# Kernel tuning notes

Hardware: AMD Instinct MI355X
Metric: run time of the kernel (lower is better)

The kernel has to match this reference:

```python
import jax, jax.numpy as jnp
import numpy as np

B, T, H, W = 2, 4, 32, 32
DINO_DIM, COG_DIM, NUM_HEADS = 768, 1920, 12
HEAD_DIM = DINO_DIM // NUM_HEADS


def _layernorm(x, g, b, eps=1e-5):
    mu = jnp.mean(x, axis=-1, keepdims=True)
    var = jnp.mean(jnp.square(x - mu), axis=-1, keepdims=True)
    return (x - mu) * jax.lax.rsqrt(var + eps) * g + b


def setup_inputs() -> dict:
    key = jax.random.key(0)
    ks = jax.random.split(key, 12)
    s_d = 1.0 / np.sqrt(DINO_DIM)
    s_c = 1.0 / np.sqrt(COG_DIM)
    return {
        "dino_query": jax.random.normal(ks[0], (B, DINO_DIM, H, W), jnp.float32),
        "cogvideo_keys": jax.random.normal(ks[1], (B, T, H, W, COG_DIM), jnp.float32),
        "temporal_weights": jax.random.uniform(ks[2], (T,), jnp.float32),
        "Wq": jax.random.normal(ks[3], (DINO_DIM, DINO_DIM), jnp.float32) * s_d,
        "bq": jnp.zeros((DINO_DIM,), jnp.float32),
        "Wk": jax.random.normal(ks[4], (COG_DIM, DINO_DIM), jnp.float32) * s_c,
        "bk": jnp.zeros((DINO_DIM,), jnp.float32),
        "Wv": jax.random.normal(ks[5], (COG_DIM, DINO_DIM), jnp.float32) * s_c,
        "bv": jnp.zeros((DINO_DIM,), jnp.float32),
        "Wo": jax.random.normal(ks[6], (DINO_DIM, DINO_DIM), jnp.float32) * s_d,
        "bo": jnp.zeros((DINO_DIM,), jnp.float32),
        "gq": jnp.ones((DINO_DIM,), jnp.float32),
        "Bq": jnp.zeros((DINO_DIM,), jnp.float32),
        "gkv": jnp.ones((COG_DIM,), jnp.float32),
        "Bkv": jnp.zeros((COG_DIM,), jnp.float32),
    }


def reference(dino_query, cogvideo_keys, temporal_weights,
              Wq, bq, Wk, bk, Wv, bv, Wo, bo, gq, Bq, gkv, Bkv):
    b, c, h, w = dino_query.shape
    t = cogvideo_keys.shape[1]
    hw, tkv = h * w, t * cogvideo_keys.shape[2] * cogvideo_keys.shape[3]

    # [B,C,H,W] -> [B,H,W,C]; project after LayerNorm
    xq = _layernorm(jnp.transpose(dino_query, (0, 2, 3, 1)), gq, Bq)
    xkv = _layernorm(cogvideo_keys, gkv, Bkv)
    q = xq @ Wq + bq                      # [B,H,W,C]
    k = xkv @ Wk + bk                     # [B,T,Hk,Wk,C]
    v = xkv @ Wv + bv

    q = q.reshape(b, hw, NUM_HEADS, HEAD_DIM).transpose(0, 2, 1, 3)    # [B,nh,HW,hd]
    k = k.reshape(b, tkv, NUM_HEADS, HEAD_DIM).transpose(0, 2, 1, 3)   # [B,nh,TKV,hd]
    v = v.reshape(b, tkv, NUM_HEADS, HEAD_DIM).transpose(0, 2, 1, 3)

    scores = jnp.einsum('bnqd,bnkd->bnqk', q, k) / np.sqrt(HEAD_DIM)   # [B,nh,HW,TKV]
    # per-key temporal weight: each of the T frames contributes HW keys
    w_key = jnp.repeat(temporal_weights, tkv // t)                     # [TKV]
    scores = scores * w_key[None, None, None, :]
    probs = jax.nn.softmax(scores, axis=-1)

    out = jnp.einsum('bnqk,bnkd->bnqd', probs, v)                      # [B,nh,HW,hd]
    out = out.transpose(0, 2, 1, 3).reshape(b, h, w, c)
    out = out @ Wo + bo
    return jnp.transpose(out, (0, 3, 1, 2))                            # [B,C,H,W]
```

## Files before the change

### kernel.cpp

```cpp
#include <hip/hip_runtime.h>
#include <hip/hip_bf16.h>
#include <math.h>

#define BB   2
#define HWl  1024
#define DINO 768
#define COG  1920
#define NHh  12
#define TKV  4096
#define MQ   (BB*HWl)
#define MKV  (BB*TKV)
#define NSPL 4
#define ROWS_PER_SPLIT (BB*NHh*HWl)

typedef __attribute__((ext_vector_type(8))) short bf16x8;
typedef __attribute__((ext_vector_type(4))) float f32x4;

__device__ __forceinline__ unsigned short f2bf_bits(float f) {
    __hip_bfloat16 h = __float2bfloat16(f);
    return *reinterpret_cast<unsigned short*>(&h);
}

__device__ __forceinline__ void glds16(const __hip_bfloat16* g, __hip_bfloat16* l) {
    __builtin_amdgcn_global_load_lds((const __attribute__((address_space(1))) void*)g,
                                     (__attribute__((address_space(3))) void*)l, 16, 0, 0);
}

__global__ __launch_bounds__(256) void prep1(const float* __restrict__ dino,
                                             const float* __restrict__ cog,
                                             const float* __restrict__ gkv, const float* __restrict__ Bkv,
                                             const float* __restrict__ Wq, const float* __restrict__ Wk,
                                             const float* __restrict__ Wv, const float* __restrict__ Wo,
                                             float* __restrict__ xqT,
                                             __hip_bfloat16* __restrict__ xkv,
                                             __hip_bfloat16* WqT, __hip_bfloat16* WkvT, __hip_bfloat16* WoT) {
    int bid = blockIdx.x, tid = threadIdx.x;
    if (bid < 2048) {
        const int W = COG, W4 = W >> 2, NC = 8;
        int row = bid * 4 + (tid >> 6), lane = tid & 63;
        const float4* xr = (const float4*)(cog + (size_t)row * W);
        const float4* g4 = (const float4*)gkv;
        const float4* b4 = (const float4*)Bkv;
        float4 v[NC];
        float s = 0.f, ss = 0.f;
        #pragma unroll
        for (int i = 0; i < NC; ++i) {
            int c = lane + i * 64;
            float4 t = (c < W4) ? xr[c] : (float4){0.f, 0.f, 0.f, 0.f};
            v[i] = t;
            s  += t.x + t.y + t.z + t.w;
            ss += t.x * t.x + t.y * t.y + t.z * t.z + t.w * t.w;
        }
        #pragma unroll
        for (int off = 1; off < 64; off <<= 1) {
            s  += __shfl_xor(s, off);
            ss += __shfl_xor(ss, off);
        }
        float mu = s / W;
        float rstd = rsqrtf(ss / W - mu * mu + 1e-5f);
        ushort4* yr = (ushort4*)(xkv + (size_t)row * W);
        #pragma unroll
        for (int i = 0; i < NC; ++i) {
            int c = lane + i * 64;
            if (c < W4) {
                float4 t = v[i];
                float4 gg = g4[c], bb = b4[c];
                ushort4 o;
                o.x = f2bf_bits((t.x - mu) * rstd * gg.x + bb.x);
                o.y = f2bf_bits((t.y - mu) * rstd * gg.y + bb.y);
                o.z = f2bf_bits((t.z - mu) * rstd * gg.z + bb.z);
                o.w = f2bf_bits((t.w - mu) * rstd * gg.w + bb.w);
                yr[c] = o;
            }
        }
    } else if (bid < 2432) {
        int t = bid - 2048;
        int h0 = (t & 15) * 64;
        int c0 = ((t >> 4) % 12) * 64;
        int b = t / 192;
        __shared__ float T[64][65];
        #pragma unroll
        for (int i = 0; i < 16; ++i) {
            int idx = tid + i * 256;
            int c = idx >> 6, h = idx & 63;
            T[c][h] = dino[((size_t)b * DINO + c0 + c) * HWl + h0 + h];
        }
        __syncthreads();
        #pragma unroll
        for (int i = 0; i < 16; ++i) {
            int idx = tid + i * 256;
            int r = idx >> 6, c = idx & 63;
            xqT[((size_t)b * HWl + h0 + r) * DINO + c0 + c] = T[c][r];
        }
    } else {
        int bid2 = bid - 2432;
        int mid = bid2 / 1440, r = bid2 % 1440;
        int k0 = (r % 60) * 32, n0 = (r / 60) * 32;
        const float* src = (mid == 0) ? Wq : (mid == 1) ? Wk : (mid == 2) ? Wv : Wo;
        __hip_bfloat16* dst;
        int rowoff = 0;
        if (mid == 0) dst = WqT;
        else if (mid == 1) dst = WkvT;
        else if (mid == 2) { dst = WkvT; rowoff = 768; }
        else dst = WoT;
        int K = (mid == 1 || mid == 2) ? COG : DINO;
        if (k0 >= K) return;
        __shared__ float T[32][33];
        #pragma unroll
        for (int i = 0; i < 4; ++i) {
            int idx = tid + i * 256;
            int rr = idx >> 5, c = idx & 31;
            T[rr][c] = src[(size_t)(k0 + rr) * DINO + n0 + c];
        }
        __syncthreads();
        #pragma unroll
        for (int i = 0; i < 4; ++i) {
            int idx = tid + i * 256;
            int rr = idx >> 5, c = idx & 31;
            dst[(size_t)(rowoff + n0 + rr) * K + k0 + c] = __float2bfloat16(T[c][rr]);
        }
    }
}

__global__ __launch_bounds__(256) void prep2(const float* __restrict__ x,
                                             const float* __restrict__ g,
                                             const float* __restrict__ be,
                                             __hip_bfloat16* __restrict__ y) {
    const int W = DINO, NC = 3;
    int row = blockIdx.x * 4 + (threadIdx.x >> 6);
    int lane = threadIdx.x & 63;
    const float4* xr = (const float4*)(x + (size_t)row * W);
    const float4* g4 = (const float4*)g;
    const float4* b4 = (const float4*)be;
    float4 v[NC];
    float s = 0.f, ss = 0.f;
    #pragma unroll
    for (int i = 0; i < NC; ++i) {
        int c = lane + i * 64;
        float4 t = xr[c];
        v[i] = t;
        s  += t.x + t.y + t.z + t.w;
        ss += t.x * t.x + t.y * t.y + t.z * t.z + t.w * t.w;
    }
    #pragma unroll
    for (int off = 1; off < 64; off <<= 1) {
        s  += __shfl_xor(s, off);
        ss += __shfl_xor(ss, off);
    }
    float mu = s / W;
    float rstd = rsqrtf(ss / W - mu * mu + 1e-5f);
    ushort4* yr = (ushort4*)(y + (size_t)row * W);
    #pragma unroll
    for (int i = 0; i < NC; ++i) {
        int c = lane + i * 64;
        float4 t = v[i];
        float4 gg = g4[c], bb = b4[c];
        ushort4 o;
        o.x = f2bf_bits((t.x - mu) * rstd * gg.x + bb.x);
        o.y = f2bf_bits((t.y - mu) * rstd * gg.y + bb.y);
        o.z = f2bf_bits((t.z - mu) * rstd * gg.z + bb.z);
        o.w = f2bf_bits((t.w - mu) * rstd * gg.w + bb.w);
        yr[c] = o;
    }
}

#define VM4 asm volatile("s_waitcnt vmcnt(4)" ::: "memory")
#define VM0 asm volatile("s_waitcnt vmcnt(0)" ::: "memory")

#define STAGE_A(d, h, tau) do { \
    int _o = (aRow + (h) * 64) * Kd + (tau) * 64 + cgo; \
    __hip_bfloat16* _dp = SM + (d) * 32768 + (h) * 8192 + wido; \
    glds16(Ag + _o, _dp); \
    glds16(Ag + _o + 128 * Kd, _dp + 4096); \
} while (0)

#define STAGE_B(d, h, tau) do { \
    int _o = (bRow + (h) * 32) * Kd + (tau) * 64 + cgo; \
    __hip_bfloat16* _dp = SM + (d) * 32768 + 16384 + (h) * 8192 + wido; \
    glds16(Bg + _o, _dp); \
    glds16(Bg + _o + 128 * Kd, _dp + 4096); \
} while (0)

#define PHASE(MH, NH, STAGE_STMT, WAIT_STMT) do { \
    const __hip_bfloat16* _Ab = SM + cur * 32768 + (MH) * 8192 + aoff; \
    const __hip_bfloat16* _Bb = SM + cur * 32768 + 16384 + (NH) * 8192 + boff; \
    bf16x8 _a[4][2], _b[2][2]; \
    _Pragma("unroll") \
    for (int i = 0; i < 4; ++i) { \
        _a[i][0] = *(const bf16x8*)(_Ab + i * 1024 + c0); \
        _a[i][1] = *(const bf16x8*)(_Ab + i * 1024 + c1); \
    } \
    _Pragma("unroll") \
    for (int j = 0; j < 2; ++j) { \
        _b[j][0] = *(const bf16x8*)(_Bb + j * 1024 + c0); \
        _b[j][1] = *(const bf16x8*)(_Bb + j * 1024 + c1); \
    } \
    STAGE_STMT; \
    WAIT_STMT; \
    __builtin_amdgcn_sched_barrier(0); \
    __builtin_amdgcn_s_barrier(); \
    __builtin_amdgcn_sched_barrier(0); \
    __builtin_amdgcn_s_setprio(1); \
    _Pragma("unroll") \
    for (int i = 0; i < 4; ++i) \
        _Pragma("unroll") \
        for (int j = 0; j < 2; ++j) { \
            f32x4 _t = acc[(MH) * 4 + i][(NH) * 2 + j]; \
            _t = __builtin_amdgcn_mfma_f32_16x16x32_bf16(_a[i][0], _b[j][0], _t, 0, 0, 0); \
            _t = __builtin_amdgcn_mfma_f32_16x16x32_bf16(_a[i][1], _b[j][1], _t, 0, 0, 0); \
            acc[(MH) * 4 + i][(NH) * 2 + j] = _t; \
        } \
    __builtin_amdgcn_s_setprio(0); \
    __builtin_amdgcn_sched_barrier(0); \
    __builtin_amdgcn_s_barrier(); \
} while (0)

__global__ __launch_bounds__(512, 2) void stage1(const __hip_bfloat16* __restrict__ xq,
                                                 const __hip_bfloat16* __restrict__ WqT,
                                                 const float* __restrict__ bq,
                                                 __hip_bfloat16* __restrict__ qb,
                                                 const __hip_bfloat16* __restrict__ xkv,
                                                 const __hip_bfloat16* __restrict__ WkvT,
                                                 const float* __restrict__ bk,
                                                 const float* __restrict__ bv,
                                                 __hip_bfloat16* __restrict__ kb,
                                                 __hip_bfloat16* __restrict__ VT) {
    __shared__ __hip_bfloat16 SM[65536];
    int bid = blockIdx.x;
    int tid = threadIdx.x;
    int wid = tid >> 6, lane = tid & 63;
    int l4 = lane & 15, lq = lane >> 4;
    int wr = wid >> 2, wc = wid & 3;
    int tr = tid >> 3;
    int cgo = ((tid & 7) ^ (tr & 7)) * 8;
    int wido = wid * 512;

    const __hip_bfloat16 *Ag, *Bg;
    int m0, n0, Kd, NT, isQ;
    if (bid < 192) {
        m0 = (bid & 31) * 256; n0 = (bid >> 5) * 256;
        Ag = xkv; Bg = WkvT; Kd = COG; NT = COG / 64; isQ = 0;
    } else {
        int t = bid - 192;
        m0 = (t & 7) * 256; n0 = (t >> 3) * 256;
        Ag = xq; Bg = WqT; Kd = DINO; NT = DINO / 64; isQ = 1;
    }

    const int aRow = m0 + tr;
    const int bRow = n0 + ((tid >> 8) << 6) + (tr & 31);
    const int aoff = (wr * 64 + l4) * 64;
    const int boff = (wc * 32 + l4) * 64;
    const int c0 = ((lq) ^ (l4 & 7)) * 8;
    const int c1 = ((4 + lq) ^ (l4 & 7)) * 8;

    f32x4 acc[8][4];
    #pragma unroll
    for (int i = 0; i < 8; ++i)
        #pragma unroll
        for (int j = 0; j < 4; ++j) acc[i][j] = (f32x4){0.f, 0.f, 0.f, 0.f};

    STAGE_A(0, 0, 0); STAGE_B(0, 0, 0); STAGE_A(0, 1, 0); STAGE_B(0, 1, 0);
    STAGE_A(1, 0, 1); STAGE_B(1, 0, 1);
    VM4;
    __builtin_amdgcn_s_barrier();

    for (int g = 0; g < NT; ++g) {
        int cur = g & 1, nxt = cur ^ 1;
        bool s1 = (g + 1 < NT), s2 = (g + 2 < NT);
        PHASE(0, 0, if (s1) STAGE_A(nxt, 1, g + 1), (void)0);
        PHASE(1, 0, if (s1) STAGE_B(nxt, 1, g + 1), (void)0);
        PHASE(0, 1, if (s2) STAGE_B(cur, 0, g + 2), (void)0);
        PHASE(1, 1, if (s2) STAGE_A(cur, 0, g + 2),
              if (s2) { VM4; } else { VM0; });
    }

    if (isQ) {
        #pragma unroll
        for (int ii = 0; ii < 8; ++ii)
            #pragma unroll
            for (int jj = 0; jj < 4; ++jj) {
                int m = m0 + wr * 128 + (ii >> 2) * 64 + (ii & 3) * 16 + lq * 4;
                int n = n0 + wc * 64 + (jj >> 1) * 32 + (jj & 1) * 16 + l4;
                float bb = bq[n];
                #pragma unroll
                for (int r = 0; r < 4; ++r)
                    qb[(size_t)(m + r) * DINO + n] = __float2bfloat16(acc[ii][jj][r] + bb);
            }
    } else if (n0 < 768) {
        #pragma unroll
        for (int ii = 0; ii < 8; ++ii)
            #pragma unroll
            for (int jj = 0; jj < 4; ++jj) {
                int m = m0 + wr * 128 + (ii >> 2) * 64 + (ii & 3) * 16 + lq * 4;
                int n = n0 + wc * 64 + (jj >> 1) * 32 + (jj & 1) * 16 + l4;
                float bb = bk[n];
                #pragma unroll
                for (int r = 0; r < 4; ++r)
                    kb[(size_t)(m + r) * DINO + n] = __float2bfloat16(acc[ii][jj][r] + bb);
            }
    } else {
        #pragma unroll
        for (int ii = 0; ii < 8; ++ii)
            #pragma unroll
            for (int jj = 0; jj < 4; ++jj) {
                int m = m0 + wr * 128 + (ii >> 2) * 64 + (ii & 3) * 16 + lq * 4;
                int nv = n0 - 768 + wc * 64 + (jj >> 1) * 32 + (jj & 1) * 16 + l4;
                float bb = bv[nv];
                #pragma unroll
                for (int r = 0; r < 4; ++r) {
                    int mm = m + r;
                    VT[((size_t)((mm >> 12) * 768 + nv)) * TKV + (mm & 4095)] =
                        __float2bfloat16(acc[ii][jj][r] + bb);
                }
            }
    }
}

__global__ __launch_bounds__(256) void gemm_o(const __hip_bfloat16* __restrict__ A,
                                              const __hip_bfloat16* __restrict__ Bt,
                                              const float* __restrict__ bias,
                                              float* __restrict__ out) {
    const int K = DINO;
    __shared__ __hip_bfloat16 As[64 * 64];
    __shared__ __hip_bfloat16 Bs[64 * 64];
    int m0 = blockIdx.x * 64, n0 = blockIdx.y * 64;
    int tid = threadIdx.x, w = tid >> 6, lane = tid & 63;
    int l4 = lane & 15, lq = lane >> 4;
    int mq = (w & 1) * 32, nq = (w >> 1) * 32;
    f32x4 acc[2][2];
    #pragma unroll
    for (int i = 0; i < 2; ++i)
        #pragma unroll
        for (int j = 0; j < 2; ++j) acc[i][j] = (f32x4){0.f, 0.f, 0.f, 0.f};

    int rr = tid >> 3;
    int gc = (tid & 7) ^ (rr & 7);
    const __hip_bfloat16* ag = A  + (size_t)(m0 + rr) * K + gc * 8;
    const __hip_bfloat16* bg = Bt + (size_t)(n0 + rr) * K + gc * 8;
    __hip_bfloat16* asl = As + (w * 8) * 64;
    __hip_bfloat16* bsl = Bs + (w * 8) * 64;
    int sws = l4 & 7;

    for (int k0 = 0; k0 < K; k0 += 64) {
        __syncthreads();
        #pragma unroll
        for (int g = 0; g < 2; ++g) {
            glds16(ag + (size_t)(g * 32) * K + k0, asl + g * 32 * 64);
            glds16(bg + (size_t)(g * 32) * K + k0, bsl + g * 32 * 64);
        }
        __syncthreads();
        #pragma unroll
        for (int h = 0; h < 2; ++h) {
            bf16x8 a[2], b[2];
            #pragma unroll
            for (int i = 0; i < 2; ++i)
                a[i] = *(const bf16x8*)(As + (mq + 16 * i + l4) * 64 + (((h * 4 + lq) ^ sws) * 8));
            #pragma unroll
            for (int j = 0; j < 2; ++j)
                b[j] = *(const bf16x8*)(Bs + (nq + 16 * j + l4) * 64 + (((h * 4 + lq) ^ sws) * 8));
            #pragma unroll
            for (int i = 0; i < 2; ++i)
                #pragma unroll
                for (int j = 0; j < 2; ++j)
                    acc[i][j] = __builtin_amdgcn_mfma_f32_16x16x32_bf16(b[j], a[i], acc[i][j], 0, 0, 0);
        }
    }
    #pragma unroll
    for (int i = 0; i < 2; ++i)
        #pragma unroll
        for (int j = 0; j < 2; ++j)
            #pragma unroll
            for (int r = 0; r < 4; ++r) {
                int n = n0 + nq + 16 * j + lq * 4 + r;
                int m = m0 + mq + 16 * i + l4;
                int b = m >> 10, hw = m & 1023;
                out[((size_t)b * DINO + n) * HWl + hw] = acc[i][j][r] + bias[n];
            }
}

__global__ __launch_bounds__(256) void attn4(const __hip_bfloat16* __restrict__ qb,
                                             const __hip_bfloat16* __restrict__ kb,
                                             const __hip_bfloat16* __restrict__ VT,
                                             const float* __restrict__ tw,
                                             __hip_bfloat16* __restrict__ Opart,
                                             float* __restrict__ lpart) {
    int bid = blockIdx.x;
    int g = bid % 96, qc = bid / 96;
    int s = g & 3, bh = g >> 2;
    int head = bh % NHh, b = bh / NHh;
    int tid = threadIdx.x, w = tid >> 6, lane = tid & 63;
    int l4 = lane & 15, lq = lane >> 4;

    __shared__ __hip_bfloat16 Ks[2 * 64 * 64];
    __shared__ __hip_bfloat16 Vs[2 * 64 * 64];
    __shared__ __hip_bfloat16 Ps[4 * 32 * 64];

    const __hip_bfloat16* qbase = qb + (size_t)(b * HWl + qc * 128 + w * 32 + l4) * DINO + head * 64;
    bf16x8 qA0 = *(const bf16x8*)(qbase + lq * 8);
    bf16x8 qA1 = *(const bf16x8*)(qbase + 32 + lq * 8);
    const __hip_bfloat16* qbase2 = qbase + (size_t)16 * DINO;
    bf16x8 qB0 = *(const bf16x8*)(qbase2 + lq * 8);
    bf16x8 qB1 = *(const bf16x8*)(qbase2 + 32 + lq * 8);

    float c = tw[s] * 0.125f * 1.44269504f;
    float l_iA = 0.f, l_iB = 0.f;
    f32x4 oA[4], oB[4];
    #pragma unroll
    for (int j = 0; j < 4; ++j) { oA[j] = (f32x4){0.f,0.f,0.f,0.f}; oB[j] = (f32x4){0.f,0.f,0.f,0.f}; }

    int rowA = w * 16 + (lane >> 3);
    int cg = (lane & 7) ^ ((lane >> 3) & 7);
    const __hip_bfloat16* kg0 = kb + (size_t)(b * TKV + s * 1024 + rowA) * DINO + head * 64 + cg * 8;
    const __hip_bfloat16* kg1 = kg0 + (size_t)8 * DINO;
    const __hip_bfloat16* vg0 = VT + (size_t)(b * 768 + head * 64 + rowA) * TKV + s * 1024 + cg * 8;
    const __hip_bfloat16* vg1 = vg0 + (size_t)8 * TKV;
    int klo0 = (w * 2 + 0) * 512, klo1 = (w * 2 + 1) * 512;

    int sw0 = (lq ^ (l4 & 7)) * 8;
    int sw1 = ((4 + lq) ^ (l4 & 7)) * 8;
    __hip_bfloat16* PsA = Ps + w * 2048 + l4 * 64;
    __hip_bfloat16* PsB = Ps + w * 2048 + (16 + l4) * 64;

    glds16(kg0, Ks + klo0);
    glds16(kg1, Ks + klo1);
    glds16(vg0, Vs + klo0);
    glds16(vg1, Vs + klo1);

    for (int kt = 0; kt < 16; ++kt) {
        int cur = (kt & 1) * 4096;
        __syncthreads();
        if (kt < 15) {
            int nxt = cur ^ 4096;
            glds16(kg0 + (size_t)(kt + 1) * 64 * DINO, Ks + nxt + klo0);
            glds16(kg1 + (size_t)(kt + 1) * 64 * DINO, Ks + nxt + klo1);
            glds16(vg0 + (kt + 1) * 64, Vs + nxt + klo0);
            glds16(vg1 + (kt + 1) * 64, Vs + nxt + klo1);
        }
        const __hip_bfloat16* Kc = Ks + cur;
        const __hip_bfloat16* Vc = Vs + cur;

        f32x4 stA[4], stB[4];
        #pragma unroll
        for (int j = 0; j < 4; ++j) {
            const __hip_bfloat16* kr = Kc + (16 * j + l4) * 64;
            bf16x8 kf0 = *(const bf16x8*)(kr + sw0);
            bf16x8 kf1 = *(const bf16x8*)(kr + sw1);
            f32x4 a = (f32x4){0.f,0.f,0.f,0.f};
            a = __builtin_amdgcn_mfma_f32_16x16x32_bf16(kf0, qA0, a, 0, 0, 0);
            a = __builtin_amdgcn_mfma_f32_16x16x32_bf16(kf1, qA1, a, 0, 0, 0);
            stA[j] = a;
            f32x4 bb = (f32x4){0.f,0.f,0.f,0.f};
            bb = __builtin_amdgcn_mfma_f32_16x16x32_bf16(kf0, qB0, bb, 0, 0, 0);
            bb = __builtin_amdgcn_mfma_f32_16x16x32_bf16(kf1, qB1, bb, 0, 0, 0);
            stB[j] = bb;
        }

        float lsA = 0.f, lsB = 0.f;
        #pragma unroll
        for (int j = 0; j < 4; ++j)
            #pragma unroll
            for (int r = 0; r < 4; ++r) {
                float eA = exp2f(stA[j][r] * c);
                float eB = exp2f(stB[j][r] * c);
                stA[j][r] = eA; lsA += eA;
                stB[j][r] = eB; lsB += eB;
            }
        lsA += __shfl_xor(lsA, 16); lsA += __shfl_xor(lsA, 32);
        lsB += __shfl_xor(lsB, 16); lsB += __shfl_xor(lsB, 32);
        l_iA += lsA; l_iB += lsB;

        #pragma unroll
        for (int j = 0; j < 4; ++j) {
            int off = (((2 * j + (lq >> 1)) ^ (l4 & 7)) << 3) + (lq & 1) * 4;
            ushort4 pA, pB;
            pA.x = f2bf_bits(stA[j][0]); pA.y = f2bf_bits(stA[j][1]);
            pA.z = f2bf_bits(stA[j][2]); pA.w = f2bf_bits(stA[j][3]);
            pB.x = f2bf_bits(stB[j][0]); pB.y = f2bf_bits(stB[j][1]);
            pB.z = f2bf_bits(stB[j][2]); pB.w = f2bf_bits(stB[j][3]);
            *(ushort4*)&PsA[off] = pA;
            *(ushort4*)&PsB[off] = pB;
        }
        bf16x8 paA0 = *(const bf16x8*)(PsA + sw0);
        bf16x8 paA1 = *(const bf16x8*)(PsA + sw1);
        bf16x8 paB0 = *(const bf16x8*)(PsB + sw0);
        bf16x8 paB1 = *(const bf16x8*)(PsB + sw1);

        #pragma unroll
        for (int j = 0; j < 4; ++j) {
            const __hip_bfloat16* vr = Vc + (16 * j + l4) * 64;
            bf16x8 vf0 = *(const bf16x8*)(vr + sw0);
            bf16x8 vf1 = *(const bf16x8*)(vr + sw1);
            oA[j] = __builtin_amdgcn_mfma_f32_16x16x32_bf16(paA0, vf0, oA[j], 0, 0, 0);
            oA[j] = __builtin_amdgcn_mfma_f32_16x16x32_bf16(paA1, vf1, oA[j], 0, 0, 0);
            oB[j] = __builtin_amdgcn_mfma_f32_16x16x32_bf16(paB0, vf0, oB[j], 0, 0, 0);
            oB[j] = __builtin_amdgcn_mfma_f32_16x16x32_bf16(paB1, vf1, oB[j], 0, 0, 0);
        }
    }

    size_t rb = (size_t)s * ROWS_PER_SPLIT + (size_t)(b * NHh + head) * HWl + qc * 128 + w * 32;
    #pragma unroll
    for (int j = 0; j < 4; ++j)
        #pragma unroll
        for (int r = 0; r < 4; ++r) {
            Opart[(rb + lq * 4 + r) * 64 + j * 16 + l4]      = __float2bfloat16(oA[j][r]);
            Opart[(rb + 16 + lq * 4 + r) * 64 + j * 16 + l4] = __float2bfloat16(oB[j][r]);
        }
    if (lq == 0) {
        lpart[rb + l4]      = l_iA;
        lpart[rb + 16 + l4] = l_iB;
    }
}

__global__ void combine(const __hip_bfloat16* __restrict__ Opart, const float* __restrict__ lpart,
                        __hip_bfloat16* __restrict__ attn) {
    int p = blockIdx.x * 4 + (threadIdx.x >> 6);
    int d = threadIdx.x & 63;
    float L = 0.f, O = 0.f;
    #pragma unroll
    for (int s = 0; s < NSPL; ++s) {
        L += lpart[(size_t)s * ROWS_PER_SPLIT + p];
        O += __bfloat162float(Opart[((size_t)s * ROWS_PER_SPLIT + p) * 64 + d]);
    }
    float res = O / L;
    int q = p & 1023;
    int bh = p >> 10;
    int head = bh % NHh, b = bh / NHh;
    attn[((size_t)(b * HWl + q)) * DINO + head * 64 + d] = __float2bfloat16(res);
}

extern "C" void kernel_launch(void* const* d_in, const int* in_sizes, int n_in,
                              void* d_out, int out_size, void* d_ws, size_t ws_size,
                              hipStream_t stream) {
    (void)in_sizes; (void)n_in; (void)out_size; (void)ws_size;
    const float* dino = (const float*)d_in[0];
    const float* cog  = (const float*)d_in[1];
    const float* tw   = (const float*)d_in[2];
    const float* Wq   = (const float*)d_in[3];
    const float* bq   = (const float*)d_in[4];
    const float* Wk   = (const float*)d_in[5];
    const float* bk   = (const float*)d_in[6];
    const float* Wv   = (const float*)d_in[7];
    const float* bv   = (const float*)d_in[8];
    const float* Wo   = (const float*)d_in[9];
    const float* bo   = (const float*)d_in[10];
    const float* gq   = (const float*)d_in[11];
    const float* Bq   = (const float*)d_in[12];
    const float* gkv  = (const float*)d_in[13];
    const float* Bkv  = (const float*)d_in[14];

    char* p = (char*)d_ws;
    float* xqT = (float*)p;                    p += (size_t)MQ * DINO * 4;
    __hip_bfloat16* xq = (__hip_bfloat16*)p;   p += (size_t)MQ * DINO * 2;
    char* alias = p;                           p += (size_t)MKV * COG * 2;
    __hip_bfloat16* xkv = (__hip_bfloat16*)alias;
    __hip_bfloat16* WqT  = (__hip_bfloat16*)p; p += (size_t)DINO * DINO * 2;
    __hip_bfloat16* WkvT = (__hip_bfloat16*)p; p += (size_t)1536 * COG * 2;
    __hip_bfloat16* WoT  = (__hip_bfloat16*)p; p += (size_t)DINO * DINO * 2;
    __hip_bfloat16* qb   = (__hip_bfloat16*)p; p += (size_t)MQ  * DINO * 2;
    __hip_bfloat16* kb   = (__hip_bfloat16*)p; p += (size_t)MKV * DINO * 2;
    __hip_bfloat16* VT   = (__hip_bfloat16*)p; p += (size_t)MKV * DINO * 2;
    __hip_bfloat16* attnb = (__hip_bfloat16*)p; p += (size_t)MQ * DINO * 2;
    __hip_bfloat16* Opart = (__hip_bfloat16*)alias;
    float* lpart = (float*)(alias + (size_t)NSPL * ROWS_PER_SPLIT * 64 * 2);

    prep1<<<8192, 256, 0, stream>>>(dino, cog, gkv, Bkv,
                                    Wq, Wk, Wv, Wo, xqT, xkv, WqT, WkvT, WoT);
    prep2<<<MQ / 4, 256, 0, stream>>>(xqT, gq, Bq, xq);
    stage1<<<216, 512, 0, stream>>>(xq, WqT, bq, qb, xkv, WkvT, bk, bv, kb, VT);
    attn4<<<BB * NHh * 8 * NSPL, 256, 0, stream>>>(qb, kb, VT, tw, Opart, lpart);
    combine<<<ROWS_PER_SPLIT / 4, 256, 0, stream>>>(Opart, lpart, attnb);
    gemm_o<<<dim3(32, 12), 256, 0, stream>>>(attnb, WoT, bo, (float*)d_out);
}
```

Before: 267.6 us.

## Restructure stage1 GEMM pipeline to reuse register fragments and halve barriers

Reworks the K-loop of the projection GEMM so that A and B fragments loaded from LDS are kept in registers and reused across the four MFMA phases (order 00,01,11,10), instead of reloading both for each phase. The per-phase trailing barrier is dropped, and the prefetch distance goes from two K-tiles to one, with adjusted vmcnt waits. This is meant to cut LDS read traffic and barrier stalls, at the cost of more live registers and a shorter prefetch lead that could expose global-load latency or introduce LDS hazards.

```diff
diff --git a/kernel.cpp b/kernel.cpp
--- a/kernel.cpp
+++ b/kernel.cpp
@@ -165,6 +165,7 @@
 }
 
 #define VM4 asm volatile("s_waitcnt vmcnt(4)" ::: "memory")
+#define VM2 asm volatile("s_waitcnt vmcnt(2)" ::: "memory")
 #define VM0 asm volatile("s_waitcnt vmcnt(0)" ::: "memory")
 
 #define STAGE_A(d, h, tau) do { \
@@ -181,22 +182,25 @@
     glds16(Bg + _o + 128 * Kd, _dp + 4096); \
 } while (0)
 
-#define PHASE(MH, NH, STAGE_STMT, WAIT_STMT) do { \
+#define LDS_A_FRAG(dst, MH) do { \
     const __hip_bfloat16* _Ab = SM + cur * 32768 + (MH) * 8192 + aoff; \
-    const __hip_bfloat16* _Bb = SM + cur * 32768 + 16384 + (NH) * 8192 + boff; \
-    bf16x8 _a[4][2], _b[2][2]; \
     _Pragma("unroll") \
     for (int i = 0; i < 4; ++i) { \
-        _a[i][0] = *(const bf16x8*)(_Ab + i * 1024 + c0); \
-        _a[i][1] = *(const bf16x8*)(_Ab + i * 1024 + c1); \
+        dst[i][0] = *(const bf16x8*)(_Ab + i * 1024 + c0); \
+        dst[i][1] = *(const bf16x8*)(_Ab + i * 1024 + c1); \
     } \
+} while (0)
+
+#define LDS_B_FRAG(dst, NH) do { \
+    const __hip_bfloat16* _Bb = SM + cur * 32768 + 16384 + (NH) * 8192 + boff; \
     _Pragma("unroll") \
     for (int j = 0; j < 2; ++j) { \
-        _b[j][0] = *(const bf16x8*)(_Bb + j * 1024 + c0); \
-        _b[j][1] = *(const bf16x8*)(_Bb + j * 1024 + c1); \
+        dst[j][0] = *(const bf16x8*)(_Bb + j * 1024 + c0); \
+        dst[j][1] = *(const bf16x8*)(_Bb + j * 1024 + c1); \
     } \
-    STAGE_STMT; \
-    WAIT_STMT; \
+} while (0)
+
+#define BARRIER_MFMA(MH, NH, af, bf) do { \
     __builtin_amdgcn_sched_barrier(0); \
     __builtin_amdgcn_s_barrier(); \
     __builtin_amdgcn_sched_barrier(0); \
@@ -206,13 +210,12 @@
         _Pragma("unroll") \
         for (int j = 0; j < 2; ++j) { \
             f32x4 _t = acc[(MH) * 4 + i][(NH) * 2 + j]; \
-            _t = __builtin_amdgcn_mfma_f32_16x16x32_bf16(_a[i][0], _b[j][0], _t, 0, 0, 0); \
-            _t = __builtin_amdgcn_mfma_f32_16x16x32_bf16(_a[i][1], _b[j][1], _t, 0, 0, 0); \
+            _t = __builtin_amdgcn_mfma_f32_16x16x32_bf16(af[i][0], bf[j][0], _t, 0, 0, 0); \
+            _t = __builtin_amdgcn_mfma_f32_16x16x32_bf16(af[i][1], bf[j][1], _t, 0, 0, 0); \
             acc[(MH) * 4 + i][(NH) * 2 + j] = _t; \
         } \
     __builtin_amdgcn_s_setprio(0); \
     __builtin_amdgcn_sched_barrier(0); \
-    __builtin_amdgcn_s_barrier(); \
 } while (0)
 
 __global__ __launch_bounds__(512, 2) void stage1(const __hip_bfloat16* __restrict__ xq,
@@ -259,19 +262,27 @@
         #pragma unroll
         for (int j = 0; j < 4; ++j) acc[i][j] = (f32x4){0.f, 0.f, 0.f, 0.f};
 
-    STAGE_A(0, 0, 0); STAGE_B(0, 0, 0); STAGE_A(0, 1, 0); STAGE_B(0, 1, 0);
-    STAGE_A(1, 0, 1); STAGE_B(1, 0, 1);
-    VM4;
+    bf16x8 a0[4][2], a1[4][2], b0[2][2], b1[2][2];
+
+    STAGE_A(0, 0, 0); STAGE_B(0, 0, 0); STAGE_B(0, 1, 0); STAGE_A(0, 1, 0);
+    VM0;
     __builtin_amdgcn_s_barrier();
 
     for (int g = 0; g < NT; ++g) {
         int cur = g & 1, nxt = cur ^ 1;
-        bool s1 = (g + 1 < NT), s2 = (g + 2 < NT);
-        PHASE(0, 0, if (s1) STAGE_A(nxt, 1, g + 1), (void)0);
-        PHASE(1, 0, if (s1) STAGE_B(nxt, 1, g + 1), (void)0);
-        PHASE(0, 1, if (s2) STAGE_B(cur, 0, g + 2), (void)0);
-        PHASE(1, 1, if (s2) STAGE_A(cur, 0, g + 2),
-              if (s2) { VM4; } else { VM0; });
+        bool s1 = (g + 1 < NT);
+        LDS_A_FRAG(a0, 0);
+        LDS_B_FRAG(b0, 0);
+        if (s1) { STAGE_A(nxt, 0, g + 1); VM4; } else { VM2; }
+        BARRIER_MFMA(0, 0, a0, b0);
+        LDS_B_FRAG(b1, 1);
+        if (s1) { STAGE_B(nxt, 0, g + 1); VM4; } else { VM0; }
+        BARRIER_MFMA(0, 1, a0, b1);
+        LDS_A_FRAG(a1, 1);
+        if (s1) { STAGE_B(nxt, 1, g + 1); }
+        BARRIER_MFMA(1, 1, a1, b1);
+        if (s1) { STAGE_A(nxt, 1, g + 1); VM4; }
+        BARRIER_MFMA(1, 0, a1, b0);
     }
 
     if (isQ) {
```

Measured after the change: 255.5 us. -4.5%, faster.
